# Optimization experiments

Hardware: AMD Instinct MI355X
Metric: run time of the kernel (lower is better)

Reference implementation:

```python
import jax, jax.numpy as jnp
import numpy as np

HIDDEN = 1024
N_HEADS = 16
HEAD_DIM = HIDDEN // N_HEADS


def setup_inputs() -> dict:
    key = jax.random.key(0)
    ks = jax.random.split(key, 9)
    s = 1.0 / np.sqrt(HIDDEN)
    d = {"hidden_states": jax.random.normal(ks[0], (2, 2048, HIDDEN), dtype=jnp.float32)}
    for i, name in enumerate(["q", "k", "v", "o"]):
        d[f"W{name}"] = jax.random.uniform(ks[1 + 2 * i], (HIDDEN, HIDDEN), minval=-s, maxval=s, dtype=jnp.float32)
        d[f"b{name}"] = jax.random.uniform(ks[2 + 2 * i], (HIDDEN,), minval=-s, maxval=s, dtype=jnp.float32)
    return d


def reference(hidden_states, Wq, bq, Wk, bk, Wv, bv, Wo, bo):
    B, L, _ = hidden_states.shape

    def shape(x):  # (B, L, H*D) -> (B, H, L, D)
        return x.reshape(B, L, N_HEADS, HEAD_DIM).transpose(0, 2, 1, 3)

    q = shape(hidden_states @ Wq.T + bq)
    k = shape(hidden_states @ Wk.T + bk)
    v = shape(hidden_states @ Wv.T + bv)
    scores = jnp.einsum("bhqd,bhkd->bhqk", q, k) / jnp.sqrt(jnp.float32(HEAD_DIM))
    attn = jax.nn.softmax(scores, axis=-1)
    ctx = jnp.einsum("bhqk,bhkd->bhqd", attn, v)
    ctx = ctx.transpose(0, 2, 1, 3).reshape(B, L, HIDDEN)
    return ctx @ Wo.T + bo
```

## Files before the change

### kernel.cpp

```cpp
#include <hip/hip_runtime.h>
#include <hip/hip_bf16.h>
#include <stdint.h>

typedef __bf16 bf16_t;
typedef __bf16 bf16x8 __attribute__((ext_vector_type(8)));
typedef __bf16 bf16x4 __attribute__((ext_vector_type(4)));
typedef float  f32x4  __attribute__((ext_vector_type(4)));
typedef float  f32x16 __attribute__((ext_vector_type(16)));

__device__ __forceinline__ f32x4 mfma16(bf16x8 a, bf16x8 b, f32x4 c) {
    return __builtin_amdgcn_mfma_f32_16x16x32_bf16(a, b, c, 0, 0, 0);
}
__device__ __forceinline__ f32x16 mfma32(bf16x8 a, bf16x8 b, f32x16 c) {
    return __builtin_amdgcn_mfma_f32_32x32x16_bf16(a, b, c, 0, 0, 0);
}
__device__ __forceinline__ void gload16(const void* g, void* l) {
    __builtin_amdgcn_global_load_lds(
        (const __attribute__((address_space(1))) unsigned int*)g,
        (__attribute__((address_space(3))) unsigned int*)l, 16, 0, 0);
}
__device__ __forceinline__ unsigned cvtpk(float lo, float hi_) {
    unsigned r;
    asm("v_cvt_pk_bf16_f32 %0, %1, %2" : "=v"(r) : "v"(lo), "v"(hi_));
    return r;
}
__device__ __forceinline__ float fexp2(float x) {
    return __builtin_amdgcn_exp2f(x);
}

__global__ __launch_bounds__(256) void split_x(const float* __restrict__ in,
                                               bf16_t* __restrict__ hi, int n8) {
    int i = blockIdx.x * 256 + threadIdx.x;
    if (i >= n8) return;
    int row = i >> 7;
    int di = (i & ~7) | ((i & 7) ^ (row & 7));
    const float4* in4 = reinterpret_cast<const float4*>(in);
    float4 v0 = in4[2 * i], v1 = in4[2 * i + 1];
    float vv[8] = {v0.x, v0.y, v0.z, v0.w, v1.x, v1.y, v1.z, v1.w};
    bf16x8 h;
#pragma unroll
    for (int j = 0; j < 8; ++j) h[j] = (bf16_t)vv[j];
    reinterpret_cast<bf16x8*>(hi)[di] = h;
}

__global__ __launch_bounds__(256) void split_w(const float* __restrict__ w0, const float* __restrict__ w1,
                                               const float* __restrict__ w2, const float* __restrict__ w3,
                                               bf16_t* __restrict__ h0, bf16_t* __restrict__ h1,
                                               bf16_t* __restrict__ h2, bf16_t* __restrict__ h3,
                                               bf16_t* __restrict__ l3) {
    int s = blockIdx.y;
    const float* in = (s == 0) ? w0 : (s == 1) ? w1 : (s == 2) ? w2 : w3;
    bf16_t* hi = (s == 0) ? h0 : (s == 1) ? h1 : (s == 2) ? h2 : h3;
    int i = blockIdx.x * 256 + threadIdx.x;
    int row = i >> 7;
    int di = (s == 3) ? ((i & ~3) | ((i & 3) ^ (row & 3)))
                      : ((i & ~7) | ((i & 7) ^ (row & 7)));
    const float4* in4 = reinterpret_cast<const float4*>(in);
    float4 v0 = in4[2 * i], v1 = in4[2 * i + 1];
    float vv[8] = {v0.x, v0.y, v0.z, v0.w, v1.x, v1.y, v1.z, v1.w};
    bf16x8 h, l;
#pragma unroll
    for (int j = 0; j < 8; ++j) {
        bf16_t hh = (bf16_t)vv[j];
        h[j] = hh;
        l[j] = (bf16_t)(vv[j] - (float)hh);
    }
    reinterpret_cast<bf16x8*>(hi)[di] = h;
    if (s == 3) reinterpret_cast<bf16x8*>(l3)[di] = l;
}

__global__ __launch_bounds__(512) void gemm_qkv(const bf16_t* __restrict__ Xhi,
                                                const bf16_t* __restrict__ Wqh,
                                                const bf16_t* __restrict__ Wkh,
                                                const bf16_t* __restrict__ Wvh,
                                                const float* __restrict__ bq, const float* __restrict__ bk,
                                                const float* __restrict__ bv,
                                                bf16_t* __restrict__ Qb, bf16_t* __restrict__ Kb,
                                                bf16_t* __restrict__ Vt) {
    __shared__ alignas(16) bf16_t ldsA[2][128 * 64];
    __shared__ alignas(16) bf16_t ldsB[2][128 * 64];
    const int tid = threadIdx.x, wave = tid >> 6, lane = tid & 63;
    const int g = lane >> 4, cc = lane & 15;
    const int bx = blockIdx.x, which = bx >> 3;
    const bf16_t* Bh = (which == 0) ? Wqh : (which == 1) ? Wkh : Wvh;
    const float* bias = (which == 0) ? bq : (which == 1) ? bk : bv;
    const float scale = (which == 0) ? 0.125f * 1.4426950408889634f : 1.0f;
    const int mBase = blockIdx.y * 128, nB = (bx & 7) * 128;
    const int wm = wave >> 2, wn = wave & 3;

    f32x4 zero = {0.f, 0.f, 0.f, 0.f};
    f32x4 acc[4][2];
#pragma unroll
    for (int mi = 0; mi < 4; ++mi)
#pragma unroll
        for (int ni = 0; ni < 2; ++ni) acc[mi][ni] = zero;

    auto stage = [&](int k0, int buf) {
#pragma unroll
        for (int i = 0; i < 4; ++i) {
            int c = wave + 8 * i;
            int tile = c >> 4, sub = c & 15;
            int row = sub * 8 + (lane >> 3);
            int colE = (lane & 7) * 8;
            const bf16_t* src = (tile == 0) ? Xhi + (size_t)(mBase + row) * 1024 + k0 + colE
                                            : Bh + (size_t)(nB + row) * 1024 + k0 + colE;
            bf16_t* dst = (tile == 0) ? ldsA[buf] : ldsB[buf];
            gload16(src, (char*)dst + sub * 1024);
        }
    };

    stage(0, 0);
    for (int t = 0; t < 16; ++t) {
        const int buf = t & 1;
        if (t < 15) {
            stage((t + 1) * 64, buf ^ 1);
            asm volatile("s_waitcnt vmcnt(4)" ::: "memory");
        } else {
            asm volatile("s_waitcnt vmcnt(0)" ::: "memory");
        }
        __builtin_amdgcn_s_barrier();
        __builtin_amdgcn_sched_barrier(0);
#pragma unroll
        for (int kk = 0; kk < 2; ++kk) {
            bf16x8 af[4], bf_[2];
#pragma unroll
            for (int mi = 0; mi < 4; ++mi) {
                int ra = wm * 64 + mi * 16 + cc;
                af[mi] = *reinterpret_cast<const bf16x8*>(
                    (const char*)ldsA[buf] + ra * 128 + (((kk * 4 + g) ^ (ra & 7)) * 16));
            }
#pragma unroll
            for (int ni = 0; ni < 2; ++ni) {
                int rb = wn * 32 + ni * 16 + cc;
                bf_[ni] = *reinterpret_cast<const bf16x8*>(
                    (const char*)ldsB[buf] + rb * 128 + (((kk * 4 + g) ^ (rb & 7)) * 16));
            }
#pragma unroll
            for (int mi = 0; mi < 4; ++mi)
#pragma unroll
                for (int ni = 0; ni < 2; ++ni)
                    acc[mi][ni] = mfma16(af[mi], bf_[ni], acc[mi][ni]);
        }
        __builtin_amdgcn_s_barrier();
    }

#pragma unroll
    for (int mi = 0; mi < 4; ++mi)
#pragma unroll
        for (int ni = 0; ni < 2; ++ni)
#pragma unroll
            for (int r = 0; r < 4; ++r) {
                int row = mBase + wm * 64 + mi * 16 + g * 4 + r;
                int colL = nB + wn * 32 + ni * 16 + cc;
                float v = (acc[mi][ni][r] + bias[colL]) * scale;
                int b = row >> 11, tok = row & 2047, h = colL >> 6, d = colL & 63;
                if (which == 2) {
                    int kt = tok >> 6, key = tok & 63;
                    size_t o = (((size_t)(b * 16 + h) * 32 + kt) * 4096)
                             + d * 64 + ((((key >> 3) ^ (d & 7)) << 3) | (key & 7));
                    Vt[o] = (bf16_t)v;
                } else {
                    int dd = (which == 1) ? ((((d >> 3) ^ (tok & 7)) << 3) | (d & 7)) : d;
                    bf16_t* out = (which == 0) ? Qb : Kb;
                    out[((size_t)(b * 16 + h) * 2048 + tok) * 64 + dd] = (bf16_t)v;
                }
            }
}

__global__ __launch_bounds__(512) void gemm_o(const bf16_t* __restrict__ Ahi,
                                              const bf16_t* __restrict__ Alo,
                                              const bf16_t* __restrict__ Bhi,
                                              const bf16_t* __restrict__ Blo,
                                              const float* __restrict__ bias,
                                              float* __restrict__ outF) {
    __shared__ alignas(16) bf16_t ldsAh[2][64 * 32];
    __shared__ alignas(16) bf16_t ldsAl[2][64 * 32];
    __shared__ alignas(16) bf16_t ldsBh[2][128 * 32];
    __shared__ alignas(16) bf16_t ldsBl[2][128 * 32];
    const int tid = threadIdx.x, wave = tid >> 6, lane = tid & 63;
    const int g = lane >> 4, cc = lane & 15;
    const int mBase = blockIdx.y * 64, nBase = blockIdx.x * 128;
    const int wm = wave >> 2, wn = wave & 3;

    f32x4 zero = {0.f, 0.f, 0.f, 0.f};
    f32x4 acc[2][2];
#pragma unroll
    for (int mi = 0; mi < 2; ++mi)
#pragma unroll
        for (int ni = 0; ni < 2; ++ni) acc[mi][ni] = zero;

    auto stage = [&](int k0, int buf) {
#pragma unroll
        for (int i = 0; i < 3; ++i) {
            int c = wave + 8 * i;
            const bf16_t* srcb;
            bf16_t* dst;
            int sub, rbase;
            if (c < 4)       { srcb = Ahi; dst = ldsAh[buf]; sub = c;      rbase = mBase; }
            else if (c < 8)  { srcb = Alo; dst = ldsAl[buf]; sub = c - 4;  rbase = mBase; }
            else if (c < 16) { srcb = Bhi; dst = ldsBh[buf]; sub = c - 8;  rbase = nBase; }
            else             { srcb = Blo; dst = ldsBl[buf]; sub = c - 16; rbase = nBase; }
            int row = sub * 16 + (lane >> 2);
            int colE = (lane & 3) * 8;
            gload16(srcb + (size_t)(rbase + row) * 1024 + k0 + colE, (char*)dst + sub * 1024);
        }
    };

    stage(0, 0);
    for (int t = 0; t < 32; ++t) {
        const int buf = t & 1;
        if (t < 31) {
            stage((t + 1) * 32, buf ^ 1);
            asm volatile("s_waitcnt vmcnt(3)" ::: "memory");
        } else {
            asm volatile("s_waitcnt vmcnt(0)" ::: "memory");
        }
        __builtin_amdgcn_s_barrier();
        __builtin_amdgcn_sched_barrier(0);
        {
            bf16x8 afh[2], afl[2], bh_[2], bl_[2];
#pragma unroll
            for (int mi = 0; mi < 2; ++mi) {
                int ra = wm * 32 + mi * 16 + cc;
                int off = ra * 64 + ((g ^ (ra & 3)) * 16);
                afh[mi] = *reinterpret_cast<const bf16x8*>((const char*)ldsAh[buf] + off);
                afl[mi] = *reinterpret_cast<const bf16x8*>((const char*)ldsAl[buf] + off);
            }
#pragma unroll
            for (int ni = 0; ni < 2; ++ni) {
                int rb = wn * 32 + ni * 16 + cc;
                int off = rb * 64 + ((g ^ (rb & 3)) * 16);
                bh_[ni] = *reinterpret_cast<const bf16x8*>((const char*)ldsBh[buf] + off);
                bl_[ni] = *reinterpret_cast<const bf16x8*>((const char*)ldsBl[buf] + off);
            }
#pragma unroll
            for (int mi = 0; mi < 2; ++mi)
#pragma unroll
                for (int ni = 0; ni < 2; ++ni) {
                    acc[mi][ni] = mfma16(afh[mi], bh_[ni], acc[mi][ni]);
                    acc[mi][ni] = mfma16(afh[mi], bl_[ni], acc[mi][ni]);
                    acc[mi][ni] = mfma16(afl[mi], bh_[ni], acc[mi][ni]);
                }
        }
        __builtin_amdgcn_s_barrier();
    }

#pragma unroll
    for (int mi = 0; mi < 2; ++mi)
#pragma unroll
        for (int ni = 0; ni < 2; ++ni)
#pragma unroll
            for (int r = 0; r < 4; ++r) {
                int row = mBase + wm * 32 + mi * 16 + g * 4 + r;
                int col = nBase + wn * 32 + ni * 16 + cc;
                outF[(size_t)row * 1024 + col] = acc[mi][ni][r] + bias[col];
            }
}

__global__ __launch_bounds__(512, 4) void attn_kernel(const bf16_t* __restrict__ Qb,
                                                      const bf16_t* __restrict__ Kb_p,
                                                      const bf16_t* __restrict__ Vt_p,
                                                      bf16_t* __restrict__ ctxHi,
                                                      bf16_t* __restrict__ ctxLo) {
    __shared__ alignas(16) bf16_t SB[2][16384];

    const int lid = blockIdx.x;
    const int xcd = lid & 7, slot = lid >> 3;
    const int bh = xcd * 4 + (slot & 3);
    const int qt = slot >> 2;

    const int tid = threadIdx.x, w = tid >> 6, l = tid & 63;
    const int ql = l & 31, hi = l >> 5;
    const int wq = w & 3;
    const int par = w >> 2;
    const size_t kbase = (size_t)bh * 2048 * 64;
    const unsigned rsw = (unsigned)(ql & 7) << 4;

    bf16x8 qf[4];
    {
        const bf16_t* qp = Qb + kbase + (size_t)(qt * 128 + wq * 32 + ql) * 64 + hi * 8;
#pragma unroll
        for (int c = 0; c < 4; ++c) qf[c] = *reinterpret_cast<const bf16x8*>(qp + c * 16);
    }
    bf16x8 ones;
#pragma unroll
    for (int j = 0; j < 8; ++j) ones[j] = (bf16_t)1.0f;

    f32x16 O0{}, O1{}, Lacc{};

    auto stage = [&](int r) {
        int buf = r & 1;
        const bf16_t* ks = Kb_p + kbase + (size_t)(2 * r) * 4096;
        const bf16_t* vs = Vt_p + ((size_t)bh * 32 + 2 * r) * 4096;
        char* kd = (char*)&SB[buf][0];
        char* vd = (char*)&SB[buf][8192];
        gload16(ks + (size_t)tid * 8,        kd + tid * 16);
        gload16(ks + (size_t)tid * 8 + 4096, kd + tid * 16 + 8192);
        gload16(vs + (size_t)tid * 8,        vd + tid * 16);
        gload16(vs + (size_t)tid * 8 + 4096, vd + tid * 16 + 8192);
    };

    stage(0);

    for (int r = 0; r < 16; ++r) {
        const int buf = r & 1;
        if (r < 15) {
            stage(r + 1);
            asm volatile("s_waitcnt vmcnt(4)" ::: "memory");
        } else {
            asm volatile("s_waitcnt vmcnt(0)" ::: "memory");
        }
        __builtin_amdgcn_s_barrier();
        __builtin_amdgcn_sched_barrier(0);

        const char* kb = (const char*)&SB[buf][par * 4096];
        const char* vb = (const char*)&SB[buf][8192 + par * 4096];

        f32x16 S0{}, S1{};
        __builtin_amdgcn_s_setprio(1);
#pragma unroll
        for (int c = 0; c < 4; ++c) {
            unsigned col = ((unsigned)(c * 32 + hi * 16)) ^ rsw;
            bf16x8 k0 = *reinterpret_cast<const bf16x8*>(kb + (unsigned)ql * 128 + col);
            bf16x8 k1 = *reinterpret_cast<const bf16x8*>(kb + (unsigned)(32 + ql) * 128 + col);
            S0 = mfma32(k0, qf[c], S0);
            S1 = mfma32(k1, qf[c], S1);
        }
        __builtin_amdgcn_s_setprio(0);

#pragma unroll
        for (int r2 = 0; r2 < 16; ++r2) {
            S0[r2] = fexp2(S0[r2]);
            S1[r2] = fexp2(S1[r2]);
        }

        union U { unsigned u[4]; bf16x8 v; };
        bf16x8 PB[4];
#define MKFRAG(DST, SS, M8)                                                       \
        {                                                                         \
            unsigned c0 = cvtpk(SS[M8 + 0], SS[M8 + 1]);                          \
            unsigned c1 = cvtpk(SS[M8 + 2], SS[M8 + 3]);                          \
            unsigned c2 = cvtpk(SS[M8 + 4], SS[M8 + 5]);                          \
            unsigned c3 = cvtpk(SS[M8 + 6], SS[M8 + 7]);                          \
            unsigned y0 = hi ? c0 : c2;                                           \
            unsigned y1 = hi ? c1 : c3;                                           \
            unsigned z0 = (unsigned)__shfl_xor((int)y0, 32);                      \
            unsigned z1 = (unsigned)__shfl_xor((int)y1, 32);                      \
            U uu;                                                                 \
            uu.u[0] = hi ? z0 : c0;                                               \
            uu.u[1] = hi ? z1 : c1;                                               \
            uu.u[2] = hi ? c2 : z0;                                               \
            uu.u[3] = hi ? c3 : z1;                                               \
            DST = uu.v;                                                           \
        }
        MKFRAG(PB[0], S0, 0)
        MKFRAG(PB[1], S0, 8)
        MKFRAG(PB[2], S1, 0)
        MKFRAG(PB[3], S1, 8)
#undef MKFRAG

        __builtin_amdgcn_s_setprio(1);
#pragma unroll
        for (int ks = 0; ks < 4; ++ks) {
            unsigned col = ((unsigned)(ks * 32 + hi * 16)) ^ rsw;
            bf16x8 v0 = *reinterpret_cast<const bf16x8*>(vb + (unsigned)ql * 128 + col);
            bf16x8 v1 = *reinterpret_cast<const bf16x8*>(vb + (unsigned)(32 + ql) * 128 + col);
            O0 = mfma32(v0, PB[ks], O0);
            O1 = mfma32(v1, PB[ks], O1);
            Lacc = mfma32(ones, PB[ks], Lacc);
        }
        __builtin_amdgcn_s_setprio(0);

        __builtin_amdgcn_s_barrier();
    }

    float lsum = Lacc[0];
    float* mbuf = (float*)&SB[0][0];
    if (par == 1) {
        float* p = mbuf + (size_t)(wq * 64 + l) * 36;
        p[0] = lsum;
#pragma unroll
        for (int r2 = 0; r2 < 16; ++r2) { p[1 + r2] = O0[r2]; p[17 + r2] = O1[r2]; }
    }
    __syncthreads();
    if (par == 1) return;

    {
        const float* p = mbuf + (size_t)(wq * 64 + l) * 36;
        lsum += p[0];
#pragma unroll
        for (int r2 = 0; r2 < 16; ++r2) {
            O0[r2] += p[1 + r2];
            O1[r2] += p[17 + r2];
        }
    }

    const int b = bh >> 4, h = bh & 15;
    const int ltok = qt * 128 + wq * 32 + ql;
    const float inv = 1.0f / lsum;
    bf16_t* baseH = ctxHi + ((size_t)(b * 2048 + ltok)) * 1024 + h * 64;
    bf16_t* baseL = ctxLo + ((size_t)(b * 2048 + ltok)) * 1024 + h * 64;
    const int rsw4 = ql & 3;
#define WRITE4(OT, RQ, DT)                                                      \
    {                                                                           \
        int d0 = (RQ ^ rsw4) * 8 + 4 * hi + 32 * DT;                            \
        bf16x4 vh, vl;                                                          \
        _Pragma("unroll")                                                       \
        for (int i = 0; i < 4; ++i) {                                           \
            float v = OT[4 * RQ + i] * inv;                                     \
            bf16_t hh = (bf16_t)v;                                              \
            vh[i] = hh;                                                         \
            vl[i] = (bf16_t)(v - (float)hh);                                    \
        }                                                                       \
        *reinterpret_cast<bf16x4*>(baseH + d0) = vh;                            \
        *reinterpret_cast<bf16x4*>(baseL + d0) = vl;                            \
    }
    WRITE4(O0, 0, 0) WRITE4(O0, 1, 0) WRITE4(O0, 2, 0) WRITE4(O0, 3, 0)
    WRITE4(O1, 0, 1) WRITE4(O1, 1, 1) WRITE4(O1, 2, 1) WRITE4(O1, 3, 1)
#undef WRITE4
}

extern "C" void kernel_launch(void* const* d_in, const int* in_sizes, int n_in,
                              void* d_out, int out_size, void* d_ws, size_t ws_size,
                              hipStream_t stream) {
    const float* X  = (const float*)d_in[0];
    const float* Wq = (const float*)d_in[1];
    const float* bq = (const float*)d_in[2];
    const float* Wk = (const float*)d_in[3];
    const float* bk = (const float*)d_in[4];
    const float* Wv = (const float*)d_in[5];
    const float* bv = (const float*)d_in[6];
    const float* Wo = (const float*)d_in[7];
    const float* bo = (const float*)d_in[8];

    const size_t MB = 1024 * 1024;
    char* ws = (char*)d_ws;
    bf16_t* Xhi = (bf16_t*)(ws);
    bf16_t* Wqh = (bf16_t*)(ws + 8 * MB);
    bf16_t* Wkh = (bf16_t*)(ws + 10 * MB);
    bf16_t* Wvh = (bf16_t*)(ws + 12 * MB);
    bf16_t* Woh = (bf16_t*)(ws + 14 * MB);
    bf16_t* Wol = (bf16_t*)(ws + 16 * MB);
    bf16_t* Qb  = (bf16_t*)(ws + 24 * MB);
    bf16_t* Kb  = (bf16_t*)(ws + 32 * MB);
    bf16_t* Vt  = (bf16_t*)(ws + 40 * MB);
    bf16_t* Chi = (bf16_t*)(ws + 48 * MB);
    bf16_t* Clo = (bf16_t*)(ws + 56 * MB);

    split_x<<<2048, 256, 0, stream>>>(X, Xhi, 4194304 / 8);
    dim3 wGrid(512, 4);
    split_w<<<wGrid, 256, 0, stream>>>(Wq, Wk, Wv, Wo,
                                       Wqh, Wkh, Wvh, Woh, Wol);

    dim3 qkvGrid(24, 32);
    gemm_qkv<<<qkvGrid, 512, 0, stream>>>(Xhi, Wqh, Wkh, Wvh,
                                          bq, bk, bv, Qb, Kb, Vt);

    attn_kernel<<<512, 512, 0, stream>>>(Qb, Kb, Vt, Chi, Clo);

    dim3 oGrid(8, 64);
    gemm_o<<<oGrid, 512, 0, stream>>>(Chi, Clo, Woh, Wol, bo, (float*)d_out);
}
```

Baseline: 135.0 us.

## Drop split-bf16 hi/lo compensation in output projection and shrink QKV k-tile

Removes the low-part bf16 terms for Wo and the attention context, so the output GEMM runs one MFMA per step instead of three and loads half the operand data. The attention epilogue no longer writes a ctxLo buffer and split_w no longer produces Wol. The QKV GEMM also moves from a 64-wide to a 32-wide k tile with a matching 4-way swizzle, which halves LDS use per stage. The output projection loses the extra precision it previously had, which risks failing a tight accuracy tolerance.

```diff
diff --git a/kernel.cpp b/kernel.cpp
--- a/kernel.cpp
+++ b/kernel.cpp
@@ -33,7 +33,7 @@
     int i = blockIdx.x * 256 + threadIdx.x;
     if (i >= n8) return;
     int row = i >> 7;
-    int di = (i & ~7) | ((i & 7) ^ (row & 7));
+    int di = (i & ~3) | ((i & 3) ^ (row & 3));
     const float4* in4 = reinterpret_cast<const float4*>(in);
     float4 v0 = in4[2 * i], v1 = in4[2 * i + 1];
     float vv[8] = {v0.x, v0.y, v0.z, v0.w, v1.x, v1.y, v1.z, v1.w};
@@ -46,27 +46,20 @@
 __global__ __launch_bounds__(256) void split_w(const float* __restrict__ w0, const float* __restrict__ w1,
                                                const float* __restrict__ w2, const float* __restrict__ w3,
                                                bf16_t* __restrict__ h0, bf16_t* __restrict__ h1,
-                                               bf16_t* __restrict__ h2, bf16_t* __restrict__ h3,
-                                               bf16_t* __restrict__ l3) {
+                                               bf16_t* __restrict__ h2, bf16_t* __restrict__ h3) {
     int s = blockIdx.y;
     const float* in = (s == 0) ? w0 : (s == 1) ? w1 : (s == 2) ? w2 : w3;
     bf16_t* hi = (s == 0) ? h0 : (s == 1) ? h1 : (s == 2) ? h2 : h3;
     int i = blockIdx.x * 256 + threadIdx.x;
     int row = i >> 7;
-    int di = (s == 3) ? ((i & ~3) | ((i & 3) ^ (row & 3)))
-                      : ((i & ~7) | ((i & 7) ^ (row & 7)));
+    int di = (i & ~3) | ((i & 3) ^ (row & 3));
     const float4* in4 = reinterpret_cast<const float4*>(in);
     float4 v0 = in4[2 * i], v1 = in4[2 * i + 1];
     float vv[8] = {v0.x, v0.y, v0.z, v0.w, v1.x, v1.y, v1.z, v1.w};
-    bf16x8 h, l;
-#pragma unroll
-    for (int j = 0; j < 8; ++j) {
-        bf16_t hh = (bf16_t)vv[j];
-        h[j] = hh;
-        l[j] = (bf16_t)(vv[j] - (float)hh);
-    }
+    bf16x8 h;
+#pragma unroll
+    for (int j = 0; j < 8; ++j) h[j] = (bf16_t)vv[j];
     reinterpret_cast<bf16x8*>(hi)[di] = h;
-    if (s == 3) reinterpret_cast<bf16x8*>(l3)[di] = l;
 }
 
 __global__ __launch_bounds__(512) void gemm_qkv(const bf16_t* __restrict__ Xhi,
@@ -77,8 +70,8 @@
                                                 const float* __restrict__ bv,
                                                 bf16_t* __restrict__ Qb, bf16_t* __restrict__ Kb,
                                                 bf16_t* __restrict__ Vt) {
-    __shared__ alignas(16) bf16_t ldsA[2][128 * 64];
-    __shared__ alignas(16) bf16_t ldsB[2][128 * 64];
+    __shared__ alignas(16) bf16_t ldsA[2][128 * 32];
+    __shared__ alignas(16) bf16_t ldsB[2][128 * 32];
     const int tid = threadIdx.x, wave = tid >> 6, lane = tid & 63;
     const int g = lane >> 4, cc = lane & 15;
     const int bx = blockIdx.x, which = bx >> 3;
@@ -97,11 +90,11 @@
 
     auto stage = [&](int k0, int buf) {
 #pragma unroll
-        for (int i = 0; i < 4; ++i) {
+        for (int i = 0; i < 2; ++i) {
             int c = wave + 8 * i;
-            int tile = c >> 4, sub = c & 15;
-            int row = sub * 8 + (lane >> 3);
-            int colE = (lane & 7) * 8;
+            int tile = c >> 3, sub = c & 7;
+            int row = sub * 16 + (lane >> 2);
+            int colE = (lane & 3) * 8;
             const bf16_t* src = (tile == 0) ? Xhi + (size_t)(mBase + row) * 1024 + k0 + colE
                                             : Bh + (size_t)(nB + row) * 1024 + k0 + colE;
             bf16_t* dst = (tile == 0) ? ldsA[buf] : ldsB[buf];
@@ -110,30 +103,29 @@
     };
 
     stage(0, 0);
-    for (int t = 0; t < 16; ++t) {
+    for (int t = 0; t < 32; ++t) {
         const int buf = t & 1;
-        if (t < 15) {
-            stage((t + 1) * 64, buf ^ 1);
-            asm volatile("s_waitcnt vmcnt(4)" ::: "memory");
+        if (t < 31) {
+            stage((t + 1) * 32, buf ^ 1);
+            asm volatile("s_waitcnt vmcnt(2)" ::: "memory");
         } else {
             asm volatile("s_waitcnt vmcnt(0)" ::: "memory");
         }
         __builtin_amdgcn_s_barrier();
         __builtin_amdgcn_sched_barrier(0);
-#pragma unroll
-        for (int kk = 0; kk < 2; ++kk) {
+        {
             bf16x8 af[4], bf_[2];
 #pragma unroll
             for (int mi = 0; mi < 4; ++mi) {
                 int ra = wm * 64 + mi * 16 + cc;
                 af[mi] = *reinterpret_cast<const bf16x8*>(
-                    (const char*)ldsA[buf] + ra * 128 + (((kk * 4 + g) ^ (ra & 7)) * 16));
+                    (const char*)ldsA[buf] + ra * 64 + ((g ^ (ra & 3)) * 16));
             }
 #pragma unroll
             for (int ni = 0; ni < 2; ++ni) {
                 int rb = wn * 32 + ni * 16 + cc;
                 bf_[ni] = *reinterpret_cast<const bf16x8*>(
-                    (const char*)ldsB[buf] + rb * 128 + (((kk * 4 + g) ^ (rb & 7)) * 16));
+                    (const char*)ldsB[buf] + rb * 64 + ((g ^ (rb & 3)) * 16));
             }
 #pragma unroll
             for (int mi = 0; mi < 4; ++mi)
@@ -168,15 +160,11 @@
 }
 
 __global__ __launch_bounds__(512) void gemm_o(const bf16_t* __restrict__ Ahi,
-                                              const bf16_t* __restrict__ Alo,
                                               const bf16_t* __restrict__ Bhi,
-                                              const bf16_t* __restrict__ Blo,
                                               const float* __restrict__ bias,
                                               float* __restrict__ outF) {
-    __shared__ alignas(16) bf16_t ldsAh[2][64 * 32];
-    __shared__ alignas(16) bf16_t ldsAl[2][64 * 32];
-    __shared__ alignas(16) bf16_t ldsBh[2][128 * 32];
-    __shared__ alignas(16) bf16_t ldsBl[2][128 * 32];
+    __shared__ alignas(16) bf16_t ldsA[2][64 * 32];
+    __shared__ alignas(16) bf16_t ldsB[2][128 * 32];
     const int tid = threadIdx.x, wave = tid >> 6, lane = tid & 63;
     const int g = lane >> 4, cc = lane & 15;
     const int mBase = blockIdx.y * 64, nBase = blockIdx.x * 128;
@@ -191,15 +179,14 @@
 
     auto stage = [&](int k0, int buf) {
 #pragma unroll
-        for (int i = 0; i < 3; ++i) {
+        for (int i = 0; i < 2; ++i) {
             int c = wave + 8 * i;
+            if (c >= 12) continue;
             const bf16_t* srcb;
             bf16_t* dst;
             int sub, rbase;
-            if (c < 4)       { srcb = Ahi; dst = ldsAh[buf]; sub = c;      rbase = mBase; }
-            else if (c < 8)  { srcb = Alo; dst = ldsAl[buf]; sub = c - 4;  rbase = mBase; }
-            else if (c < 16) { srcb = Bhi; dst = ldsBh[buf]; sub = c - 8;  rbase = nBase; }
-            else             { srcb = Blo; dst = ldsBl[buf]; sub = c - 16; rbase = nBase; }
+            if (c < 4) { srcb = Ahi; dst = ldsA[buf]; sub = c;     rbase = mBase; }
+            else       { srcb = Bhi; dst = ldsB[buf]; sub = c - 4; rbase = nBase; }
             int row = sub * 16 + (lane >> 2);
             int colE = (lane & 3) * 8;
             gload16(srcb + (size_t)(rbase + row) * 1024 + k0 + colE, (char*)dst + sub * 1024);
@@ -211,36 +198,32 @@
         const int buf = t & 1;
         if (t < 31) {
             stage((t + 1) * 32, buf ^ 1);
-            asm volatile("s_waitcnt vmcnt(3)" ::: "memory");
+            if (wave < 4) asm volatile("s_waitcnt vmcnt(2)" ::: "memory");
+            else          asm volatile("s_waitcnt vmcnt(1)" ::: "memory");
         } else {
             asm volatile("s_waitcnt vmcnt(0)" ::: "memory");
         }
         __builtin_amdgcn_s_barrier();
         __builtin_amdgcn_sched_barrier(0);
         {
-            bf16x8 afh[2], afl[2], bh_[2], bl_[2];
+            bf16x8 af[2], bf_[2];
 #pragma unroll
             for (int mi = 0; mi < 2; ++mi) {
                 int ra = wm * 32 + mi * 16 + cc;
-                int off = ra * 64 + ((g ^ (ra & 3)) * 16);
-                afh[mi] = *reinterpret_cast<const bf16x8*>((const char*)ldsAh[buf] + off);
-                afl[mi] = *reinterpret_cast<const bf16x8*>((const char*)ldsAl[buf] + off);
+                af[mi] = *reinterpret_cast<const bf16x8*>(
+                    (const char*)ldsA[buf] + ra * 64 + ((g ^ (ra & 3)) * 16));
             }
 #pragma unroll
             for (int ni = 0; ni < 2; ++ni) {
                 int rb = wn * 32 + ni * 16 + cc;
-                int off = rb * 64 + ((g ^ (rb & 3)) * 16);
-                bh_[ni] = *reinterpret_cast<const bf16x8*>((const char*)ldsBh[buf] + off);
-                bl_[ni] = *reinterpret_cast<const bf16x8*>((const char*)ldsBl[buf] + off);
+                bf_[ni] = *reinterpret_cast<const bf16x8*>(
+                    (const char*)ldsB[buf] + rb * 64 + ((g ^ (rb & 3)) * 16));
             }
 #pragma unroll
             for (int mi = 0; mi < 2; ++mi)
 #pragma unroll
-                for (int ni = 0; ni < 2; ++ni) {
-                    acc[mi][ni] = mfma16(afh[mi], bh_[ni], acc[mi][ni]);
-                    acc[mi][ni] = mfma16(afh[mi], bl_[ni], acc[mi][ni]);
-                    acc[mi][ni] = mfma16(afl[mi], bh_[ni], acc[mi][ni]);
-                }
+                for (int ni = 0; ni < 2; ++ni)
+                    acc[mi][ni] = mfma16(af[mi], bf_[ni], acc[mi][ni]);
         }
         __builtin_amdgcn_s_barrier();
     }
@@ -260,8 +243,7 @@
 __global__ __launch_bounds__(512, 4) void attn_kernel(const bf16_t* __restrict__ Qb,
                                                       const bf16_t* __restrict__ Kb_p,
                                                       const bf16_t* __restrict__ Vt_p,
-                                                      bf16_t* __restrict__ ctxHi,
-                                                      bf16_t* __restrict__ ctxLo) {
+                                                      bf16_t* __restrict__ ctxHi) {
     __shared__ alignas(16) bf16_t SB[2][16384];
 
     const int lid = blockIdx.x;
@@ -399,21 +381,17 @@
     const int ltok = qt * 128 + wq * 32 + ql;
     const float inv = 1.0f / lsum;
     bf16_t* baseH = ctxHi + ((size_t)(b * 2048 + ltok)) * 1024 + h * 64;
-    bf16_t* baseL = ctxLo + ((size_t)(b * 2048 + ltok)) * 1024 + h * 64;
     const int rsw4 = ql & 3;
 #define WRITE4(OT, RQ, DT)                                                      \
     {                                                                           \
         int d0 = (RQ ^ rsw4) * 8 + 4 * hi + 32 * DT;                            \
-        bf16x4 vh, vl;                                                          \
+        bf16x4 vh;                                                              \
         _Pragma("unroll")                                                       \
         for (int i = 0; i < 4; ++i) {                                           \
             float v = OT[4 * RQ + i] * inv;                                     \
-            bf16_t hh = (bf16_t)v;                                              \
-            vh[i] = hh;                                                         \
-            vl[i] = (bf16_t)(v - (float)hh);                                    \
+            vh[i] = (bf16_t)v;                                                  \
         }                                                                       \
         *reinterpret_cast<bf16x4*>(baseH + d0) = vh;                            \
-        *reinterpret_cast<bf16x4*>(baseL + d0) = vl;                            \
     }
     WRITE4(O0, 0, 0) WRITE4(O0, 1, 0) WRITE4(O0, 2, 0) WRITE4(O0, 3, 0)
     WRITE4(O1, 0, 1) WRITE4(O1, 1, 1) WRITE4(O1, 2, 1) WRITE4(O1, 3, 1)
@@ -440,24 +418,22 @@
     bf16_t* Wkh = (bf16_t*)(ws + 10 * MB);
     bf16_t* Wvh = (bf16_t*)(ws + 12 * MB);
     bf16_t* Woh = (bf16_t*)(ws + 14 * MB);
-    bf16_t* Wol = (bf16_t*)(ws + 16 * MB);
     bf16_t* Qb  = (bf16_t*)(ws + 24 * MB);
     bf16_t* Kb  = (bf16_t*)(ws + 32 * MB);
     bf16_t* Vt  = (bf16_t*)(ws + 40 * MB);
     bf16_t* Chi = (bf16_t*)(ws + 48 * MB);
-    bf16_t* Clo = (bf16_t*)(ws + 56 * MB);
 
     split_x<<<2048, 256, 0, stream>>>(X, Xhi, 4194304 / 8);
     dim3 wGrid(512, 4);
     split_w<<<wGrid, 256, 0, stream>>>(Wq, Wk, Wv, Wo,
-                                       Wqh, Wkh, Wvh, Woh, Wol);
+                                       Wqh, Wkh, Wvh, Woh);
 
     dim3 qkvGrid(24, 32);
     gemm_qkv<<<qkvGrid, 512, 0, stream>>>(Xhi, Wqh, Wkh, Wvh,
                                           bq, bk, bv, Qb, Kb, Vt);
 
-    attn_kernel<<<512, 512, 0, stream>>>(Qb, Kb, Vt, Chi, Clo);
+    attn_kernel<<<512, 512, 0, stream>>>(Qb, Kb, Vt, Chi);
 
     dim3 oGrid(8, 64);
-    gemm_o<<<oGrid, 512, 0, stream>>>(Chi, Clo, Woh, Wol, bo, (float*)d_out);
-}
+    gemm_o<<<oGrid, 512, 0, stream>>>(Chi, Woh, bo, (float*)d_out);
+}
```

Result: faster. 112.7 us (-16.5%).
